# Optimization experiments

Hardware: AMD Instinct MI355X
Metric: run time of the kernel (lower is better)

Reference implementation:

```python
import jax, jax.numpy as jnp
import numpy as np

N, D, K = 16384, 2048, 1000

def setup_inputs() -> dict:
    key = jax.random.key(0)
    k1, k2 = jax.random.split(key)
    feats = jax.random.normal(k1, (N, D), dtype=jnp.float32)
    initc = jax.random.normal(k2, (K, D + 1), dtype=jnp.float32)
    labelset = jnp.arange(K, dtype=jnp.int64)
    return {"feats": feats, "initc": initc, "labelset": labelset}

def reference(feats, initc, labelset):
    # cosine branch: append ones column, then L2-normalize rows
    f = jnp.concatenate([feats, jnp.ones((feats.shape[0], 1), feats.dtype)], axis=1)  # [N, D+1]
    f = f / jnp.linalg.norm(f, axis=1, keepdims=True)
    c = initc[labelset]  # [L, D+1]
    # cdist (euclidean) via ||f||^2 + ||c||^2 - 2 f.c
    d2 = (jnp.sum(f * f, axis=1)[:, None]
          + jnp.sum(c * c, axis=1)[None, :]
          - 2.0 * (f @ c.T))
    dd = jnp.sqrt(jnp.maximum(d2, 0.0))  # [N, L]
    pred = jnp.argmin(dd, axis=1)
    return labelset[pred]
```

## Files before the change

kernel.cpp:

```cpp
#include <hip/hip_runtime.h>
#include <math.h>

#define N_ROWS 16384
#define DIM    2048
#define K_CENT 1000
#define KPAD   1024
#define CDIM   2049

#define WS_AH   ((size_t)0)
#define WS_AL   ((size_t)67108864)
#define WS_BH   ((size_t)134217728)
#define WS_BL   ((size_t)138412032)
#define WS_RN   ((size_t)142606336)
#define WS_CN2  ((size_t)142671872)
#define WS_CL   ((size_t)142675968)
#define WS_PV   ((size_t)142680064)
#define WS_PI   ((size_t)143728640)
#define WS_NEED ((size_t)144777216)

typedef __attribute__((ext_vector_type(8))) short bf16x8;
typedef __attribute__((ext_vector_type(4))) float f32x4;

__device__ __forceinline__ unsigned short f2bf(float x){
  unsigned int u = __float_as_uint(x);
  u += 0x7fffu + ((u >> 16) & 1u);
  return (unsigned short)(u >> 16);
}
__device__ __forceinline__ float bf2f(unsigned short h){
  return __uint_as_float(((unsigned int)h) << 16);
}

typedef const __attribute__((address_space(1))) void gv_t;
typedef __attribute__((address_space(3))) void lv_t;
__device__ __forceinline__ void gload16(const void* g, void* l){
  __builtin_amdgcn_global_load_lds((gv_t*)g, (lv_t*)l, 16, 0, 0);
}

__global__ __launch_bounds__(256) void prep_feats(const float* __restrict__ feats,
    unsigned short* __restrict__ Ah, unsigned short* __restrict__ Al,
    float* __restrict__ rnorm){
  const int row = blockIdx.x, t = threadIdx.x;
  const float4* p4 = (const float4*)(feats + (size_t)row * DIM);
  float4 v0 = p4[t], v1 = p4[t + 256];
  float e0[4] = {v0.x, v0.y, v0.z, v0.w};
  float e1[4] = {v1.x, v1.y, v1.z, v1.w};
  float s = 0.f;
  unsigned short h0[4], l0[4], h1[4], l1[4];
  #pragma unroll
  for (int q = 0; q < 4; ++q){
    s = fmaf(e0[q], e0[q], s); s = fmaf(e1[q], e1[q], s);
    unsigned short h = f2bf(e0[q]); h0[q] = h; l0[q] = f2bf(e0[q] - bf2f(h));
    h = f2bf(e1[q]); h1[q] = h; l1[q] = f2bf(e1[q] - bf2f(h));
  }
  *(ushort4*)(Ah + (size_t)row*DIM + t*4)        = make_ushort4(h0[0],h0[1],h0[2],h0[3]);
  *(ushort4*)(Ah + (size_t)row*DIM + (t+256)*4)  = make_ushort4(h1[0],h1[1],h1[2],h1[3]);
  *(ushort4*)(Al + (size_t)row*DIM + t*4)        = make_ushort4(l0[0],l0[1],l0[2],l0[3]);
  *(ushort4*)(Al + (size_t)row*DIM + (t+256)*4)  = make_ushort4(l1[0],l1[1],l1[2],l1[3]);
  #pragma unroll
  for (int mm = 1; mm < 64; mm <<= 1) s += __shfl_xor(s, mm, 64);
  __shared__ float wsm[4];
  if ((t & 63) == 0) wsm[t >> 6] = s;
  __syncthreads();
  if (t == 0) rnorm[row] = 1.0f / sqrtf(wsm[0]+wsm[1]+wsm[2]+wsm[3] + 1.0f);
}

__global__ __launch_bounds__(256) void prep_cent(const float* __restrict__ initc,
    unsigned short* __restrict__ Bh, unsigned short* __restrict__ Bl,
    float* __restrict__ cn2, float* __restrict__ cl){
  const int j = blockIdx.x, t = threadIdx.x;
  __shared__ float wsm[4];
  if (j < K_CENT){
    const float* p = initc + (size_t)j * CDIM;
    float s = 0.f;
    for (int i = t; i < CDIM; i += 256){
      float x = p[i];
      s = fmaf(x, x, s);
      if (i < DIM){
        unsigned short h = f2bf(x);
        Bh[(size_t)j*DIM + i] = h;
        Bl[(size_t)j*DIM + i] = f2bf(x - bf2f(h));
      } else {
        cl[j] = x;
      }
    }
    #pragma unroll
    for (int mm = 1; mm < 64; mm <<= 1) s += __shfl_xor(s, mm, 64);
    if ((t & 63) == 0) wsm[t >> 6] = s;
    __syncthreads();
    if (t == 0) cn2[j] = wsm[0] + wsm[1] + wsm[2] + wsm[3];
  } else {
    for (int i = t; i < DIM; i += 256){
      Bh[(size_t)j*DIM + i] = 0;
      Bl[(size_t)j*DIM + i] = 0;
    }
    if (t == 0){ cn2[j] = INFINITY; cl[j] = 0.f; }
  }
}

__global__ __launch_bounds__(256) void dist_mfma(
    const unsigned short* __restrict__ Ah, const unsigned short* __restrict__ Al,
    const unsigned short* __restrict__ Bh, const unsigned short* __restrict__ Bl,
    const float* __restrict__ rnorm, const float* __restrict__ cn2,
    const float* __restrict__ cl, float* __restrict__ pval, int* __restrict__ pidx){
  __shared__ char smem[32768];
  const int t = threadIdx.x;
  const int l = t & 63;
  const int w = t >> 6;
  const int wr = w >> 1, wc = w & 1;
  const int rowBase = blockIdx.x * 128, colBase = blockIdx.y * 128;
  const int kb = l >> 4, lr = l & 15;

  f32x4 acc[4][4];
  #pragma unroll
  for (int m = 0; m < 4; ++m)
    #pragma unroll
    for (int n = 0; n < 4; ++n)
      #pragma unroll
      for (int q = 0; q < 4; ++q) acc[m][n][q] = 0.f;

  int aOff[4], bOff[4];
  #pragma unroll
  for (int m = 0; m < 4; ++m) aOff[m] = kb*2048 + (wr*64 + m*16 + lr)*16;
  #pragma unroll
  for (int n = 0; n < 4; ++n) bOff[n] = kb*2048 + (wc*64 + n*16 + lr)*16;

  const int r0 = t & 127,        kb0 = t >> 7;
  const int r1 = (t+256) & 127,  kb1 = (t+256) >> 7;
  const size_t gA0 = (size_t)(rowBase + r0)*DIM + kb0*8;
  const size_t gA1 = (size_t)(rowBase + r1)*DIM + kb1*8;
  const size_t gB0 = (size_t)(colBase + r0)*DIM + kb0*8;
  const size_t gB1 = (size_t)(colBase + r1)*DIM + kb1*8;
  const int ld0 = t*16, ld1 = (t+256)*16;

  for (int k0 = 0; k0 < DIM; k0 += 32){
    gload16(Ah + gA0 + k0, smem + ld0);
    gload16(Ah + gA1 + k0, smem + ld1);
    gload16(Al + gA0 + k0, smem + 8192  + ld0);
    gload16(Al + gA1 + k0, smem + 8192  + ld1);
    gload16(Bh + gB0 + k0, smem + 16384 + ld0);
    gload16(Bh + gB1 + k0, smem + 16384 + ld1);
    gload16(Bl + gB0 + k0, smem + 24576 + ld0);
    gload16(Bl + gB1 + k0, smem + 24576 + ld1);
    __syncthreads();
    bf16x8 ah[4], al[4];
    #pragma unroll
    for (int m = 0; m < 4; ++m){
      ah[m] = *(const bf16x8*)(smem + aOff[m]);
      al[m] = *(const bf16x8*)(smem + 8192 + aOff[m]);
    }
    #pragma unroll
    for (int n = 0; n < 4; ++n){
      bf16x8 bh = *(const bf16x8*)(smem + 16384 + bOff[n]);
      bf16x8 bl = *(const bf16x8*)(smem + 24576 + bOff[n]);
      #pragma unroll
      for (int m = 0; m < 4; ++m){
        acc[m][n] = __builtin_amdgcn_mfma_f32_16x16x32_bf16(ah[m], bh, acc[m][n], 0, 0, 0);
        acc[m][n] = __builtin_amdgcn_mfma_f32_16x16x32_bf16(ah[m], bl, acc[m][n], 0, 0, 0);
        acc[m][n] = __builtin_amdgcn_mfma_f32_16x16x32_bf16(al[m], bh, acc[m][n], 0, 0, 0);
      }
    }
    __syncthreads();
  }

  float c2v[4], clv[4];
  #pragma unroll
  for (int n = 0; n < 4; ++n){
    int col = colBase + wc*64 + n*16 + lr;
    c2v[n] = cn2[col]; clv[n] = cl[col];
  }
  const int g4 = (l >> 4) * 4;
  #pragma unroll
  for (int m = 0; m < 4; ++m){
    int rbase = rowBase + wr*64 + m*16 + g4;
    #pragma unroll
    for (int q = 0; q < 4; ++q){
      float rn = rnorm[rbase + q];
      float bestv = INFINITY; int besti = 0x7fffffff;
      #pragma unroll
      for (int n = 0; n < 4; ++n){
        float v = c2v[n] - 2.0f * rn * (acc[m][n][q] + clv[n]);
        int ci = colBase + wc*64 + n*16 + lr;
        if (v < bestv){ bestv = v; besti = ci; }
      }
      #pragma unroll
      for (int mm = 1; mm < 16; mm <<= 1){
        float ov = __shfl_xor(bestv, mm, 64);
        int   oi = __shfl_xor(besti, mm, 64);
        if (ov < bestv || (ov == bestv && oi < besti)){ bestv = ov; besti = oi; }
      }
      if (lr == 0){
        int row = rbase + q;
        pval[row*16 + blockIdx.y*2 + wc] = bestv;
        pidx[row*16 + blockIdx.y*2 + wc] = besti;
      }
    }
  }
}

template<int NT>
__global__ __launch_bounds__(256) void argmin_final(const float* __restrict__ pval,
    const int* __restrict__ pidx, const int* __restrict__ labels,
    int* __restrict__ out){
  const int i = blockIdx.x * 256 + threadIdx.x;
  float bestv = INFINITY; int besti = 0x7fffffff;
  #pragma unroll
  for (int s = 0; s < NT; ++s){
    float v = pval[i*NT + s]; int ix = pidx[i*NT + s];
    if (v < bestv || (v == bestv && ix < besti)){ bestv = v; besti = ix; }
  }
  out[i] = labels[besti];
}

__global__ __launch_bounds__(256) void rnorm_kernel(const float* __restrict__ feats,
                                                    float* __restrict__ rnorm) {
    const int row = blockIdx.x;
    const int t = threadIdx.x;
    const float4* p4 = (const float4*)(feats + (size_t)row * DIM);
    float4 v0 = p4[t];
    float4 v1 = p4[t + 256];
    float s = v0.x*v0.x + v0.y*v0.y + v0.z*v0.z + v0.w*v0.w
            + v1.x*v1.x + v1.y*v1.y + v1.z*v1.z + v1.w*v1.w;
    #pragma unroll
    for (int m = 1; m < 64; m <<= 1) s += __shfl_xor(s, m, 64);
    __shared__ float ws[4];
    if ((t & 63) == 0) ws[t >> 6] = s;
    __syncthreads();
    if (t == 0) {
        float tot = ws[0] + ws[1] + ws[2] + ws[3] + 1.0f;
        rnorm[row] = 1.0f / sqrtf(tot);
    }
}

__global__ __launch_bounds__(256) void cn2_kernel(const float* __restrict__ initc,
                                                  float* __restrict__ cn2) {
    const int j = blockIdx.x;
    const int t = threadIdx.x;
    const float* p = initc + (size_t)j * CDIM;
    float s = 0.f;
    for (int i = t; i < CDIM; i += 256) { float v = p[i]; s = fmaf(v, v, s); }
    #pragma unroll
    for (int m = 1; m < 64; m <<= 1) s += __shfl_xor(s, m, 64);
    __shared__ float ws[4];
    if ((t & 63) == 0) ws[t >> 6] = s;
    __syncthreads();
    if (t == 0) cn2[j] = ws[0] + ws[1] + ws[2] + ws[3];
}

__global__ __launch_bounds__(256) void dist_kernel(const float* __restrict__ feats,
                                                   const float* __restrict__ initc,
                                                   const float* __restrict__ rnorm,
                                                   const float* __restrict__ cn2,
                                                   float* __restrict__ pval,
                                                   int* __restrict__ pidx) {
    __shared__ __align__(16) float As[16][128 + 4];
    __shared__ __align__(16) float Bs[16][128 + 4];
    const int bm = blockIdx.x;
    const int bn = blockIdx.y;
    const int t  = threadIdx.x;
    const int tx = t & 15;
    const int ty = t >> 4;
    const int rowBase  = bm * 128;
    const int centBase = bn * 128;
    float acc[8][8];
    #pragma unroll
    for (int i = 0; i < 8; ++i)
        #pragma unroll
        for (int j = 0; j < 8; ++j) acc[i][j] = 0.f;
    const int ar  = t >> 2;
    const int ac4 = (t & 3) << 2;
    const int bc  = t >> 4;
    const int bcol = t & 15;
    auto cidx = [&](int j) { return (j < 4) ? (tx * 4 + j) : (64 + tx * 4 + (j - 4)); };
    for (int k0 = 0; k0 < DIM; k0 += 16) {
        #pragma unroll
        for (int p = 0; p < 2; ++p) {
            int row = p * 64 + ar;
            const float4 v = *(const float4*)(feats + (size_t)(rowBase + row) * DIM + k0 + ac4);
            As[ac4 + 0][row] = v.x;
            As[ac4 + 1][row] = v.y;
            As[ac4 + 2][row] = v.z;
            As[ac4 + 3][row] = v.w;
        }
        #pragma unroll
        for (int p = 0; p < 8; ++p) {
            int cent = p * 16 + bc;
            int gj = centBase + cent;
            Bs[bcol][cent] = (gj < K_CENT) ? initc[(size_t)gj * CDIM + k0 + bcol] : 0.f;
        }
        __syncthreads();
        #pragma unroll
        for (int kk = 0; kk < 16; ++kk) {
            float a[8], b[8];
            *(float4*)&a[0] = *(const float4*)&As[kk][ty * 8];
            *(float4*)&a[4] = *(const float4*)&As[kk][ty * 8 + 4];
            *(float4*)&b[0] = *(const float4*)&Bs[kk][tx * 4];
            *(float4*)&b[4] = *(const float4*)&Bs[kk][64 + tx * 4];
            #pragma unroll
            for (int i = 0; i < 8; ++i)
                #pragma unroll
                for (int j = 0; j < 8; ++j)
                    acc[i][j] = fmaf(a[i], b[j], acc[i][j]);
        }
        __syncthreads();
    }
    float rn[8];
    #pragma unroll
    for (int i = 0; i < 8; ++i) rn[i] = rnorm[rowBase + ty * 8 + i];
    float cle[8], c2[8];
    #pragma unroll
    for (int j = 0; j < 8; ++j) {
        int gj = centBase + cidx(j);
        cle[j] = (gj < K_CENT) ? initc[(size_t)gj * CDIM + DIM] : 0.f;
        c2[j] = (gj < K_CENT) ? cn2[gj] : INFINITY;
    }
    #pragma unroll
    for (int i = 0; i < 8; ++i) {
        float bestv = INFINITY;
        int   besti = 0x7fffffff;
        #pragma unroll
        for (int j = 0; j < 8; ++j) {
            int gj = centBase + cidx(j);
            float v = (gj < K_CENT) ? (c2[j] - 2.0f * rn[i] * (acc[i][j] + cle[j])) : INFINITY;
            if (v < bestv) { bestv = v; besti = gj; }
        }
        #pragma unroll
        for (int m = 1; m < 16; m <<= 1) {
            float ov = __shfl_xor(bestv, m, 64);
            int   oi = __shfl_xor(besti, m, 64);
            if (ov < bestv || (ov == bestv && oi < besti)) { bestv = ov; besti = oi; }
        }
        if (tx == 0) {
            int row = rowBase + ty * 8 + i;
            pval[row * 8 + bn] = bestv;
            pidx[row * 8 + bn] = besti;
        }
    }
}

extern "C" void kernel_launch(void* const* d_in, const int* in_sizes, int n_in,
                              void* d_out, int out_size, void* d_ws, size_t ws_size,
                              hipStream_t stream) {
    const float* feats  = (const float*)d_in[0];
    const float* initc  = (const float*)d_in[1];
    const int*   labels = (const int*)d_in[2];
    int* out = (int*)d_out;
    char* ws = (char*)d_ws;

    if (ws_size >= WS_NEED) {
        unsigned short* Ah = (unsigned short*)(ws + WS_AH);
        unsigned short* Al = (unsigned short*)(ws + WS_AL);
        unsigned short* Bh = (unsigned short*)(ws + WS_BH);
        unsigned short* Bl = (unsigned short*)(ws + WS_BL);
        float* rn  = (float*)(ws + WS_RN);
        float* c2  = (float*)(ws + WS_CN2);
        float* clp = (float*)(ws + WS_CL);
        float* pv  = (float*)(ws + WS_PV);
        int*   pi  = (int*)  (ws + WS_PI);

        prep_feats<<<N_ROWS, 256, 0, stream>>>(feats, Ah, Al, rn);
        prep_cent<<<KPAD, 256, 0, stream>>>(initc, Bh, Bl, c2, clp);
        dim3 grid(N_ROWS / 128, KPAD / 128);
        dist_mfma<<<grid, 256, 0, stream>>>(Ah, Al, Bh, Bl, rn, c2, clp, pv, pi);
        argmin_final<16><<<N_ROWS / 256, 256, 0, stream>>>(pv, pi, labels, out);
    } else {
        float* rnorm = (float*)(ws);
        float* cn2   = (float*)(ws + 65536);
        float* pval  = (float*)(ws + 73728);
        int*   pidx  = (int*)  (ws + 73728 + 524288);

        rnorm_kernel<<<N_ROWS, 256, 0, stream>>>(feats, rnorm);
        cn2_kernel<<<K_CENT, 256, 0, stream>>>(initc, cn2);
        dim3 grid(N_ROWS / 128, 8);
        dist_kernel<<<grid, 256, 0, stream>>>(feats, initc, rnorm, cn2, pval, pidx);
        argmin_final<8><<<N_ROWS / 256, 256, 0, stream>>>(pval, pidx, labels, out);
    }
}
```

Baseline: 513.9 us.

## Switch distance GEMM to 32x32x16 MFMA with 128x256 tiles and vectorized prep

The distance kernel now uses 32x32x16 bf16 MFMA instructions and a 128x256 block tile, so each block covers a quarter of the centroids. This halves the grid's column dimension and the number of partial argmin slots per row, and raises data reuse per LDS load, at the cost of more accumulator registers and 48KB of LDS. The epilogue folds the norm scaling into one FMA via a precomputed 0.5*||f||, and the centroid norm now includes the last column. The prep kernels write 16-byte vector stores, with centroid rows staged through LDS.

```diff
diff --git a/kernel.cpp b/kernel.cpp
--- a/kernel.cpp
+++ b/kernel.cpp
@@ -15,11 +15,12 @@
 #define WS_CN2  ((size_t)142671872)
 #define WS_CL   ((size_t)142675968)
 #define WS_PV   ((size_t)142680064)
-#define WS_PI   ((size_t)143728640)
-#define WS_NEED ((size_t)144777216)
-
-typedef __attribute__((ext_vector_type(8))) short bf16x8;
-typedef __attribute__((ext_vector_type(4))) float f32x4;
+#define WS_PI   ((size_t)143204352)
+#define WS_NEED ((size_t)143728640)
+
+typedef __attribute__((ext_vector_type(8)))  short          bf16x8;
+typedef __attribute__((ext_vector_type(16))) float          f32x16;
+typedef __attribute__((ext_vector_type(8)))  unsigned short u16x8;
 
 __device__ __forceinline__ unsigned short f2bf(float x){
   unsigned int u = __float_as_uint(x);
@@ -38,61 +39,69 @@
 
 __global__ __launch_bounds__(256) void prep_feats(const float* __restrict__ feats,
     unsigned short* __restrict__ Ah, unsigned short* __restrict__ Al,
-    float* __restrict__ rnorm){
+    float* __restrict__ i2r){
   const int row = blockIdx.x, t = threadIdx.x;
   const float4* p4 = (const float4*)(feats + (size_t)row * DIM);
-  float4 v0 = p4[t], v1 = p4[t + 256];
-  float e0[4] = {v0.x, v0.y, v0.z, v0.w};
-  float e1[4] = {v1.x, v1.y, v1.z, v1.w};
+  float4 u0 = p4[2*t], u1 = p4[2*t + 1];
+  float e[8] = {u0.x,u0.y,u0.z,u0.w,u1.x,u1.y,u1.z,u1.w};
   float s = 0.f;
-  unsigned short h0[4], l0[4], h1[4], l1[4];
-  #pragma unroll
-  for (int q = 0; q < 4; ++q){
-    s = fmaf(e0[q], e0[q], s); s = fmaf(e1[q], e1[q], s);
-    unsigned short h = f2bf(e0[q]); h0[q] = h; l0[q] = f2bf(e0[q] - bf2f(h));
-    h = f2bf(e1[q]); h1[q] = h; l1[q] = f2bf(e1[q] - bf2f(h));
-  }
-  *(ushort4*)(Ah + (size_t)row*DIM + t*4)        = make_ushort4(h0[0],h0[1],h0[2],h0[3]);
-  *(ushort4*)(Ah + (size_t)row*DIM + (t+256)*4)  = make_ushort4(h1[0],h1[1],h1[2],h1[3]);
-  *(ushort4*)(Al + (size_t)row*DIM + t*4)        = make_ushort4(l0[0],l0[1],l0[2],l0[3]);
-  *(ushort4*)(Al + (size_t)row*DIM + (t+256)*4)  = make_ushort4(l1[0],l1[1],l1[2],l1[3]);
+  u16x8 hv, lv;
+  #pragma unroll
+  for (int q = 0; q < 8; ++q){
+    s = fmaf(e[q], e[q], s);
+    unsigned short h = f2bf(e[q]);
+    hv[q] = h; lv[q] = f2bf(e[q] - bf2f(h));
+  }
+  *(u16x8*)(Ah + (size_t)row*DIM + t*8) = hv;
+  *(u16x8*)(Al + (size_t)row*DIM + t*8) = lv;
   #pragma unroll
   for (int mm = 1; mm < 64; mm <<= 1) s += __shfl_xor(s, mm, 64);
   __shared__ float wsm[4];
   if ((t & 63) == 0) wsm[t >> 6] = s;
   __syncthreads();
-  if (t == 0) rnorm[row] = 1.0f / sqrtf(wsm[0]+wsm[1]+wsm[2]+wsm[3] + 1.0f);
+  if (t == 0){
+    float tot = wsm[0]+wsm[1]+wsm[2]+wsm[3] + 1.0f;
+    i2r[row] = 0.5f * sqrtf(tot);
+  }
 }
 
 __global__ __launch_bounds__(256) void prep_cent(const float* __restrict__ initc,
     unsigned short* __restrict__ Bh, unsigned short* __restrict__ Bl,
     float* __restrict__ cn2, float* __restrict__ cl){
   const int j = blockIdx.x, t = threadIdx.x;
+  __shared__ float rowbuf[DIM];
   __shared__ float wsm[4];
   if (j < K_CENT){
     const float* p = initc + (size_t)j * CDIM;
     float s = 0.f;
-    for (int i = t; i < CDIM; i += 256){
-      float x = p[i];
+    #pragma unroll
+    for (int i = 0; i < 8; ++i){
+      float x = p[t + i*256];
+      rowbuf[t + i*256] = x;
       s = fmaf(x, x, s);
-      if (i < DIM){
-        unsigned short h = f2bf(x);
-        Bh[(size_t)j*DIM + i] = h;
-        Bl[(size_t)j*DIM + i] = f2bf(x - bf2f(h));
-      } else {
-        cl[j] = x;
-      }
     }
     #pragma unroll
     for (int mm = 1; mm < 64; mm <<= 1) s += __shfl_xor(s, mm, 64);
     if ((t & 63) == 0) wsm[t >> 6] = s;
     __syncthreads();
-    if (t == 0) cn2[j] = wsm[0] + wsm[1] + wsm[2] + wsm[3];
+    if (t == 0){
+      float xl = p[DIM];
+      cl[j] = xl;
+      cn2[j] = wsm[0]+wsm[1]+wsm[2]+wsm[3] + xl*xl;
+    }
+    u16x8 hv, lv;
+    #pragma unroll
+    for (int q = 0; q < 8; ++q){
+      float x = rowbuf[t*8 + q];
+      unsigned short h = f2bf(x);
+      hv[q] = h; lv[q] = f2bf(x - bf2f(h));
+    }
+    *(u16x8*)(Bh + (size_t)j*DIM + t*8) = hv;
+    *(u16x8*)(Bl + (size_t)j*DIM + t*8) = lv;
   } else {
-    for (int i = t; i < DIM; i += 256){
-      Bh[(size_t)j*DIM + i] = 0;
-      Bl[(size_t)j*DIM + i] = 0;
-    }
+    u16x8 z = (u16x8)0;
+    *(u16x8*)(Bh + (size_t)j*DIM + t*8) = z;
+    *(u16x8*)(Bl + (size_t)j*DIM + t*8) = z;
     if (t == 0){ cn2[j] = INFINITY; cl[j] = 0.f; }
   }
 }
@@ -100,63 +109,60 @@
 __global__ __launch_bounds__(256) void dist_mfma(
     const unsigned short* __restrict__ Ah, const unsigned short* __restrict__ Al,
     const unsigned short* __restrict__ Bh, const unsigned short* __restrict__ Bl,
-    const float* __restrict__ rnorm, const float* __restrict__ cn2,
+    const float* __restrict__ i2r, const float* __restrict__ cn2,
     const float* __restrict__ cl, float* __restrict__ pval, int* __restrict__ pidx){
-  __shared__ char smem[32768];
+  __shared__ char smem[49152];
   const int t = threadIdx.x;
-  const int l = t & 63;
-  const int w = t >> 6;
+  const int l = t & 63, w = t >> 6;
   const int wr = w >> 1, wc = w & 1;
-  const int rowBase = blockIdx.x * 128, colBase = blockIdx.y * 128;
-  const int kb = l >> 4, lr = l & 15;
-
-  f32x4 acc[4][4];
-  #pragma unroll
-  for (int m = 0; m < 4; ++m)
+  const int rowBase = blockIdx.x * 128, colBase = blockIdx.y * 256;
+
+  f32x16 acc[2][4];
+  #pragma unroll
+  for (int m = 0; m < 2; ++m)
     #pragma unroll
     for (int n = 0; n < 4; ++n)
       #pragma unroll
-      for (int q = 0; q < 4; ++q) acc[m][n][q] = 0.f;
-
-  int aOff[4], bOff[4];
-  #pragma unroll
-  for (int m = 0; m < 4; ++m) aOff[m] = kb*2048 + (wr*64 + m*16 + lr)*16;
-  #pragma unroll
-  for (int n = 0; n < 4; ++n) bOff[n] = kb*2048 + (wc*64 + n*16 + lr)*16;
-
-  const int r0 = t & 127,        kb0 = t >> 7;
-  const int r1 = (t+256) & 127,  kb1 = (t+256) >> 7;
-  const size_t gA0 = (size_t)(rowBase + r0)*DIM + kb0*8;
-  const size_t gA1 = (size_t)(rowBase + r1)*DIM + kb1*8;
-  const size_t gB0 = (size_t)(colBase + r0)*DIM + kb0*8;
-  const size_t gB1 = (size_t)(colBase + r1)*DIM + kb1*8;
-  const int ld0 = t*16, ld1 = (t+256)*16;
+      for (int q = 0; q < 16; ++q) acc[m][n][q] = 0.f;
+
+  const int ar = t & 127, akb = t >> 7;
+  const size_t gA0 = (size_t)(rowBase + ar)*DIM + akb*8;
+  const size_t gA1 = gA0 + 16;
+  const size_t gBb = (size_t)(colBase + t)*DIM;
+  const int ldA0 = t*16, ldA1 = (t+256)*16;
 
   for (int k0 = 0; k0 < DIM; k0 += 32){
-    gload16(Ah + gA0 + k0, smem + ld0);
-    gload16(Ah + gA1 + k0, smem + ld1);
-    gload16(Al + gA0 + k0, smem + 8192  + ld0);
-    gload16(Al + gA1 + k0, smem + 8192  + ld1);
-    gload16(Bh + gB0 + k0, smem + 16384 + ld0);
-    gload16(Bh + gB1 + k0, smem + 16384 + ld1);
-    gload16(Bl + gB0 + k0, smem + 24576 + ld0);
-    gload16(Bl + gB1 + k0, smem + 24576 + ld1);
-    __syncthreads();
-    bf16x8 ah[4], al[4];
-    #pragma unroll
-    for (int m = 0; m < 4; ++m){
-      ah[m] = *(const bf16x8*)(smem + aOff[m]);
-      al[m] = *(const bf16x8*)(smem + 8192 + aOff[m]);
-    }
-    #pragma unroll
-    for (int n = 0; n < 4; ++n){
-      bf16x8 bh = *(const bf16x8*)(smem + 16384 + bOff[n]);
-      bf16x8 bl = *(const bf16x8*)(smem + 24576 + bOff[n]);
-      #pragma unroll
-      for (int m = 0; m < 4; ++m){
-        acc[m][n] = __builtin_amdgcn_mfma_f32_16x16x32_bf16(ah[m], bh, acc[m][n], 0, 0, 0);
-        acc[m][n] = __builtin_amdgcn_mfma_f32_16x16x32_bf16(ah[m], bl, acc[m][n], 0, 0, 0);
-        acc[m][n] = __builtin_amdgcn_mfma_f32_16x16x32_bf16(al[m], bh, acc[m][n], 0, 0, 0);
+    gload16(Ah + gA0 + k0, smem + ldA0);
+    gload16(Ah + gA1 + k0, smem + ldA1);
+    gload16(Al + gA0 + k0, smem + 8192  + ldA0);
+    gload16(Al + gA1 + k0, smem + 8192  + ldA1);
+    #pragma unroll
+    for (int q = 0; q < 4; ++q){
+      gload16(Bh + gBb + q*8 + k0, smem + 16384 + (q*256 + t)*16);
+      gload16(Bl + gBb + q*8 + k0, smem + 32768 + (q*256 + t)*16);
+    }
+    __syncthreads();
+    #pragma unroll
+    for (int s = 0; s < 2; ++s){
+      const int kb = s*2 + (l >> 5);
+      bf16x8 ah[2], al[2];
+      #pragma unroll
+      for (int m = 0; m < 2; ++m){
+        int arow = wr*64 + m*32 + (l & 31);
+        ah[m] = *(const bf16x8*)(smem + (kb*128 + arow)*16);
+        al[m] = *(const bf16x8*)(smem + 8192 + (kb*128 + arow)*16);
+      }
+      #pragma unroll
+      for (int n = 0; n < 4; ++n){
+        int boff = (kb*256 + wc*128 + n*32 + (l & 31))*16;
+        bf16x8 bh = *(const bf16x8*)(smem + 16384 + boff);
+        bf16x8 bl = *(const bf16x8*)(smem + 32768 + boff);
+        #pragma unroll
+        for (int m = 0; m < 2; ++m){
+          acc[m][n] = __builtin_amdgcn_mfma_f32_32x32x16_bf16(ah[m], bh, acc[m][n], 0, 0, 0);
+          acc[m][n] = __builtin_amdgcn_mfma_f32_32x32x16_bf16(ah[m], bl, acc[m][n], 0, 0, 0);
+          acc[m][n] = __builtin_amdgcn_mfma_f32_32x32x16_bf16(al[m], bh, acc[m][n], 0, 0, 0);
+        }
       }
     }
     __syncthreads();
@@ -165,33 +171,31 @@
   float c2v[4], clv[4];
   #pragma unroll
   for (int n = 0; n < 4; ++n){
-    int col = colBase + wc*64 + n*16 + lr;
+    int col = colBase + wc*128 + n*32 + (l & 31);
     c2v[n] = cn2[col]; clv[n] = cl[col];
   }
-  const int g4 = (l >> 4) * 4;
-  #pragma unroll
-  for (int m = 0; m < 4; ++m){
-    int rbase = rowBase + wr*64 + m*16 + g4;
-    #pragma unroll
-    for (int q = 0; q < 4; ++q){
-      float rn = rnorm[rbase + q];
+  #pragma unroll
+  for (int m = 0; m < 2; ++m){
+    #pragma unroll
+    for (int reg = 0; reg < 16; ++reg){
+      int row = rowBase + wr*64 + m*32 + (reg & 3) + 8*(reg >> 2) + 4*(l >> 5);
+      float ir = i2r[row];
       float bestv = INFINITY; int besti = 0x7fffffff;
       #pragma unroll
       for (int n = 0; n < 4; ++n){
-        float v = c2v[n] - 2.0f * rn * (acc[m][n][q] + clv[n]);
-        int ci = colBase + wc*64 + n*16 + lr;
+        float v = fmaf(c2v[n], ir, -(acc[m][n][reg] + clv[n]));
+        int ci = colBase + wc*128 + n*32 + (l & 31);
         if (v < bestv){ bestv = v; besti = ci; }
       }
       #pragma unroll
-      for (int mm = 1; mm < 16; mm <<= 1){
+      for (int mm = 1; mm < 32; mm <<= 1){
         float ov = __shfl_xor(bestv, mm, 64);
         int   oi = __shfl_xor(besti, mm, 64);
         if (ov < bestv || (ov == bestv && oi < besti)){ bestv = ov; besti = oi; }
       }
-      if (lr == 0){
-        int row = rbase + q;
-        pval[row*16 + blockIdx.y*2 + wc] = bestv;
-        pidx[row*16 + blockIdx.y*2 + wc] = besti;
+      if ((l & 31) == 0){
+        pval[row*8 + blockIdx.y*2 + wc] = bestv;
+        pidx[row*8 + blockIdx.y*2 + wc] = besti;
       }
     }
   }
@@ -351,17 +355,17 @@
         unsigned short* Al = (unsigned short*)(ws + WS_AL);
         unsigned short* Bh = (unsigned short*)(ws + WS_BH);
         unsigned short* Bl = (unsigned short*)(ws + WS_BL);
-        float* rn  = (float*)(ws + WS_RN);
+        float* ir  = (float*)(ws + WS_RN);
         float* c2  = (float*)(ws + WS_CN2);
         float* clp = (float*)(ws + WS_CL);
         float* pv  = (float*)(ws + WS_PV);
         int*   pi  = (int*)  (ws + WS_PI);
 
-        prep_feats<<<N_ROWS, 256, 0, stream>>>(feats, Ah, Al, rn);
+        prep_feats<<<N_ROWS, 256, 0, stream>>>(feats, Ah, Al, ir);
         prep_cent<<<KPAD, 256, 0, stream>>>(initc, Bh, Bl, c2, clp);
-        dim3 grid(N_ROWS / 128, KPAD / 128);
-        dist_mfma<<<grid, 256, 0, stream>>>(Ah, Al, Bh, Bl, rn, c2, clp, pv, pi);
-        argmin_final<16><<<N_ROWS / 256, 256, 0, stream>>>(pv, pi, labels, out);
+        dim3 grid(N_ROWS / 128, KPAD / 256);
+        dist_mfma<<<grid, 256, 0, stream>>>(Ah, Al, Bh, Bl, ir, c2, clp, pv, pi);
+        argmin_final<8><<<N_ROWS / 256, 256, 0, stream>>>(pv, pi, labels, out);
     } else {
         float* rnorm = (float*)(ws);
         float* cn2   = (float*)(ws + 65536);
```

Measured after the change: 680.7 us. 32.5% more time.
